# Kernel tuning notes

Hardware: AMD Instinct MI355X
Metric: run time of the kernel (lower is better)

The kernel has to match this reference:

```python
import jax, jax.numpy as jnp
import numpy as np

N, E, CIN, COUT, KHOP = 100000, 600000, 128, 128, 3


def setup_inputs() -> dict:
    key = jax.random.key(0)
    k1, k2, k3 = jax.random.split(key, 3)
    x = jax.random.normal(k1, (N, CIN), dtype=jnp.float32)
    edge_index = jax.random.randint(k2, (2, E), 0, N, dtype=jnp.int64)
    # xavier_uniform init for weight [in, out]
    limit = float(np.sqrt(6.0 / (CIN + COUT)))
    weight = jax.random.uniform(k3, (CIN, COUT), minval=-limit, maxval=limit, dtype=jnp.float32)
    bias = jnp.zeros((COUT,), jnp.float32)
    log_scale = jnp.asarray(np.log(1.0), jnp.float32)  # init_scale = 1.0
    hop_logits = jnp.zeros((KHOP + 1,), jnp.float32)
    return {"x": x, "edge_index": edge_index, "num_nodes": N,
            "weight": weight, "bias": bias,
            "log_scale": log_scale, "hop_logits": hop_logits}


def reference(x, edge_index, num_nodes, weight, bias, log_scale, hop_logits):
    src, dst = edge_index[0], edge_index[1]
    # symmetric normalization D_src^{-1/2} A D_dst^{-1/2}, no self-loops
    ones = jnp.ones(src.shape, x.dtype)
    deg_src = jax.ops.segment_sum(ones, src, num_segments=num_nodes)
    deg_dst = jax.ops.segment_sum(ones, dst, num_segments=num_nodes)
    dsi = jnp.where(deg_src > 0, jax.lax.rsqrt(jnp.maximum(deg_src, 1.0)), 0.0)
    ddi = jnp.where(deg_dst > 0, jax.lax.rsqrt(jnp.maximum(deg_dst, 1.0)), 0.0)
    edge_weight = dsi[src] * ddi[dst]  # [E]

    s = jnp.exp(log_scale)
    alpha = jax.nn.softmax(hop_logits)  # [k_hop+1]

    wavelet_out = alpha[0] * x
    current = x
    for k in range(1, KHOP + 1):  # small fixed hop count
        # A_hat @ current : gather -> scale -> scatter-add
        current = jax.ops.segment_sum(current[src] * edge_weight[:, None], dst,
                                      num_segments=num_nodes)
        decay = jnp.exp(-s * k)
        wavelet_out = wavelet_out + alpha[k] * decay * current

    return wavelet_out @ weight + bias
```

## Files before the change

### kernel.cpp

```cpp
#include <hip/hip_runtime.h>
#include <hip/hip_bf16.h>

#define C 128

typedef short s16x8 __attribute__((ext_vector_type(8)));
typedef float f32x4 __attribute__((ext_vector_type(4)));
typedef float f32x2 __attribute__((ext_vector_type(2)));

static __device__ __forceinline__ float b2f(unsigned short u) {
    union { unsigned int i; float f; } v;
    v.i = ((unsigned int)u) << 16;
    return v.f;
}
static __device__ __forceinline__ unsigned short f2b(float f) {
    __hip_bfloat16 b = __float2bfloat16(f);
    return *reinterpret_cast<unsigned short*>(&b);
}

__global__ __launch_bounds__(256) void zero_int_kernel(int4* __restrict__ p, long n4) {
    long i = blockIdx.x * 256L + threadIdx.x;
    if (i < n4) p[i] = make_int4(0, 0, 0, 0);
}

__global__ __launch_bounds__(256) void hist_kernel(
    const int* __restrict__ ei, int E,
    int* __restrict__ degs, int* __restrict__ degd) {
    int i = blockIdx.x * 256 + threadIdx.x;
    int e0 = i * 4;
    if (e0 + 4 <= E) {
        int4 s = *(const int4*)(ei + e0);
        int4 d = *(const int4*)(ei + E + e0);
        atomicAdd(&degs[s.x], 1); atomicAdd(&degs[s.y], 1);
        atomicAdd(&degs[s.z], 1); atomicAdd(&degs[s.w], 1);
        atomicAdd(&degd[d.x], 1); atomicAdd(&degd[d.y], 1);
        atomicAdd(&degd[d.z], 1); atomicAdd(&degd[d.w], 1);
    } else {
        for (int e = e0; e < E; ++e) {
            atomicAdd(&degs[ei[e]], 1);
            atomicAdd(&degd[ei[E + e]], 1);
        }
    }
}

__global__ __launch_bounds__(256) void wt_kernel(const float* __restrict__ W,
                                                 unsigned short* __restrict__ WtB,
                                                 const float* __restrict__ log_scale,
                                                 const float* __restrict__ hop_logits,
                                                 float* __restrict__ coef) {
    int tid = blockIdx.x * 256 + threadIdx.x;
    int k = tid & 127, c = tid >> 7;
    WtB[c * 128 + k] = f2b(W[k * 128 + c]);
    if (tid == 0) {
        float s = expf(log_scale[0]);
        float m = hop_logits[0];
        for (int kk = 1; kk < 4; ++kk) m = fmaxf(m, hop_logits[kk]);
        float a[4], sum = 0.0f;
        for (int kk = 0; kk < 4; ++kk) { a[kk] = expf(hop_logits[kk] - m); sum += a[kk]; }
        for (int kk = 0; kk < 4; ++kk) coef[kk] = (a[kk] / sum) * expf(-s * (float)kk);
    }
}

__global__ __launch_bounds__(256) void rpscan_kernel(const int* __restrict__ degd,
                                                     int* __restrict__ rp,
                                                     int* __restrict__ cursor,
                                                     int* __restrict__ gctr, int N) {
    __shared__ int sm[256];
    __shared__ int base_sm;
    int t = threadIdx.x;
    int i = blockIdx.x * 256 + t;
    int v = (i < N) ? degd[i] : 0;
    sm[t] = v;
    __syncthreads();
    for (int off = 1; off < 256; off <<= 1) {
        int add = (t >= off) ? sm[t - off] : 0;
        __syncthreads();
        sm[t] += add;
        __syncthreads();
    }
    if (t == 255) base_sm = atomicAdd(gctr, sm[255]);
    __syncthreads();
    if (i < N) {
        int r = base_sm + sm[t] - v;
        rp[i] = r;
        cursor[i] = r;
    }
}

__global__ __launch_bounds__(256) void scatter_kernel(const int* __restrict__ ei, int E,
                                                      int* __restrict__ cursor,
                                                      const int* __restrict__ degs,
                                                      int2* __restrict__ csr) {
    int i = blockIdx.x * 256 + threadIdx.x;
    int e0 = i * 4;
    if (e0 + 4 <= E) {
        int4 s = *(const int4*)(ei + e0);
        int4 d = *(const int4*)(ei + E + e0);
        float w0 = rsqrtf((float)degs[s.x]);
        float w1 = rsqrtf((float)degs[s.y]);
        float w2 = rsqrtf((float)degs[s.z]);
        float w3 = rsqrtf((float)degs[s.w]);
        int p0 = atomicAdd(&cursor[d.x], 1);
        int p1 = atomicAdd(&cursor[d.y], 1);
        int p2 = atomicAdd(&cursor[d.z], 1);
        int p3 = atomicAdd(&cursor[d.w], 1);
        csr[p0] = make_int2(s.x, __float_as_int(w0));
        csr[p1] = make_int2(s.y, __float_as_int(w1));
        csr[p2] = make_int2(s.z, __float_as_int(w2));
        csr[p3] = make_int2(s.w, __float_as_int(w3));
    } else {
        for (int e = e0; e < E; ++e) {
            int s = ei[e];
            int d = ei[E + e];
            float w = rsqrtf((float)degs[s]);
            int pos = atomicAdd(&cursor[d], 1);
            csr[pos] = make_int2(s, __float_as_int(w));
        }
    }
}

__global__ __launch_bounds__(256) void conv8_kernel(const float* __restrict__ x,
                                                    unsigned int* __restrict__ x8, long n4) {
    long i = blockIdx.x * 256L + threadIdx.x;
    if (i >= n4) return;
    float4 v = ((const float4*)x)[i];
    int r = __builtin_amdgcn_cvt_pk_fp8_f32(v.x, v.y, 0, false);
    r = __builtin_amdgcn_cvt_pk_fp8_f32(v.z, v.w, r, true);
    x8[i] = (unsigned int)r;
}

__global__ __launch_bounds__(256) void pull8_kernel(
    const int* __restrict__ rp, const int* __restrict__ degd,
    const int2* __restrict__ csr,
    const unsigned short* __restrict__ src8,
    unsigned short* __restrict__ dst8, int N) {
    int wid = (int)((blockIdx.x * 256L + threadIdx.x) >> 6);
    if (wid >= N) return;
    int lane = threadIdx.x & 63;
    int beg = __builtin_amdgcn_readfirstlane(rp[wid]);
    int cnt = __builtin_amdgcn_readfirstlane(degd[wid]);
    float sx = 0.f, sy = 0.f;
    if (cnt > 0) {
        for (int j = 0; j < cnt; j += 8) {
            int   idx[8];
            float wt[8];
            #pragma unroll
            for (int i = 0; i < 8; ++i) {
                int jj = j + i;
                bool ok = jj < cnt;
                int2 e = csr[beg + (ok ? jj : 0)];
                idx[i] = e.x;
                wt[i] = ok ? __int_as_float(e.y) : 0.0f;
            }
            unsigned short u[8];
            #pragma unroll
            for (int i = 0; i < 8; ++i) u[i] = src8[(long)idx[i] * 64 + lane];
            #pragma unroll
            for (int i = 0; i < 8; ++i) {
                f32x2 v = __builtin_amdgcn_cvt_pk_f32_fp8((int)u[i], false);
                sx += wt[i] * v[0];
                sy += wt[i] * v[1];
            }
        }
        float dv = rsqrtf((float)cnt);
        sx *= dv; sy *= dv;
    }
    int pk = __builtin_amdgcn_cvt_pk_fp8_f32(sx, sy, 0, false);
    dst8[(long)wid * 64 + lane] = (unsigned short)pk;
}

__global__ __launch_bounds__(256) void pull3c8_kernel(
    const int* __restrict__ rp, const int* __restrict__ degd,
    const int2* __restrict__ csr,
    const unsigned short* __restrict__ h2_8,
    const float* __restrict__ x,
    const unsigned short* __restrict__ h1_8,
    const float* __restrict__ coef,
    unsigned int* __restrict__ hc, int N) {
    int wid = (int)((blockIdx.x * 256L + threadIdx.x) >> 6);
    if (wid >= N) return;
    int lane = threadIdx.x & 63;
    int beg = __builtin_amdgcn_readfirstlane(rp[wid]);
    int cnt = __builtin_amdgcn_readfirstlane(degd[wid]);
    float sx = 0.f, sy = 0.f;
    if (cnt > 0) {
        for (int j = 0; j < cnt; j += 8) {
            int   idx[8];
            float wt[8];
            #pragma unroll
            for (int i = 0; i < 8; ++i) {
                int jj = j + i;
                bool ok = jj < cnt;
                int2 e = csr[beg + (ok ? jj : 0)];
                idx[i] = e.x;
                wt[i] = ok ? __int_as_float(e.y) : 0.0f;
            }
            unsigned short u[8];
            #pragma unroll
            for (int i = 0; i < 8; ++i) u[i] = h2_8[(long)idx[i] * 64 + lane];
            #pragma unroll
            for (int i = 0; i < 8; ++i) {
                f32x2 v = __builtin_amdgcn_cvt_pk_f32_fp8((int)u[i], false);
                sx += wt[i] * v[0];
                sy += wt[i] * v[1];
            }
        }
        float dv = rsqrtf((float)cnt);
        sx *= dv; sy *= dv;
    }
    float c0 = coef[0], c1 = coef[1], c2 = coef[2], c3 = coef[3];
    long rb = (long)wid * 64 + lane;
    float2 xv = *(const float2*)(x + (long)wid * C + lane * 2);
    f32x2 v1 = __builtin_amdgcn_cvt_pk_f32_fp8((int)h1_8[rb], false);
    f32x2 v2 = __builtin_amdgcn_cvt_pk_f32_fp8((int)h2_8[rb], false);
    float f0 = c0 * xv.x + c1 * v1[0] + c2 * v2[0] + c3 * sx;
    float f1 = c0 * xv.y + c1 * v1[1] + c2 * v2[1] + c3 * sy;
    hc[rb] = (unsigned int)f2b(f0) | ((unsigned int)f2b(f1) << 16);
}

__global__ __launch_bounds__(256) void gemm_kernel(
    const unsigned short* __restrict__ hc,
    const unsigned short* __restrict__ WtB,
    const float* __restrict__ bias,
    float* __restrict__ out, int N) {
    __shared__ unsigned short Wl[128 * 136];
    int t = threadIdx.x;

    #pragma unroll
    for (int i = 0; i < 8; ++i) {
        int ch = t + i * 256;
        int r = ch >> 4;
        int ko = (ch & 15) * 8;
        *(s16x8*)(Wl + r * 136 + ko) = *(const s16x8*)(WtB + r * 128 + ko);
    }
    __syncthreads();

    int wave = t >> 6, lane = t & 63;
    int lsel = lane & 15;
    int lk   = (lane >> 4) * 8;
    int arow = blockIdx.x * 64 + wave * 16 + lsel;
    bool rok = arow < N;
    long rbase = (long)arow * C;

    f32x4 acc[8];
    #pragma unroll
    for (int i = 0; i < 8; ++i) acc[i] = (f32x4){0.f, 0.f, 0.f, 0.f};

    #pragma unroll
    for (int ks = 0; ks < 4; ++ks) {
        int k0 = ks * 32 + lk;
        s16x8 a = rok ? *(const s16x8*)(hc + rbase + k0) : (s16x8)0;
        #pragma unroll
        for (int cf = 0; cf < 8; ++cf) {
            s16x8 b = *(const s16x8*)(Wl + (cf * 16 + lsel) * 136 + k0);
            acc[cf] = __builtin_amdgcn_mfma_f32_16x16x32_bf16(a, b, acc[cf], 0, 0, 0);
        }
    }

    int orow0 = blockIdx.x * 64 + wave * 16 + (lane >> 4) * 4;
    #pragma unroll
    for (int cf = 0; cf < 8; ++cf) {
        int ocol = cf * 16 + lsel;
        float bv = bias[ocol];
        #pragma unroll
        for (int r = 0; r < 4; ++r) {
            int orow = orow0 + r;
            if (orow < N) out[(long)orow * C + ocol] = acc[cf][r] + bv;
        }
    }
}

extern "C" void kernel_launch(void* const* d_in, const int* in_sizes, int n_in,
                              void* d_out, int out_size, void* d_ws, size_t ws_size,
                              hipStream_t stream) {
    const float* x          = (const float*)d_in[0];
    const int*   ei         = (const int*)d_in[1];
    const float* W          = (const float*)d_in[3];
    const float* bias       = (const float*)d_in[4];
    const float* log_scale  = (const float*)d_in[5];
    const float* hop_logits = (const float*)d_in[6];
    float* out = (float*)d_out;

    int N = in_sizes[0] / C;
    int E = in_sizes[1] / 2;

    char* ws = (char*)d_ws;
    size_t f8b = (size_t)N * C;
    unsigned short* x8  = (unsigned short*)ws;
    unsigned short* h18 = (unsigned short*)(ws + f8b);
    unsigned short* h28 = (unsigned short*)(ws + 2 * f8b);
    unsigned short* hc  = (unsigned short*)(ws + 3 * f8b);
    int2*  csr     = (int2*)(ws + 5 * f8b);
    int*   degs    = (int*)(csr + E);
    int*   degd    = degs + N;
    int*   gctr    = degd + N;
    int*   rp      = gctr + 16;
    int*   cursor  = rp + N;
    float* coef    = (float*)(cursor + N);
    unsigned short* WtB = (unsigned short*)(coef + 4);

    int eb4 = (E / 4 + 255) / 256 + 1;
    int nbk = (N + 255) / 256;
    int pull_blocks = (int)(((long)N * 64 + 255) / 256);

    long zn4 = (2L * N + 16 + 3) / 4;
    zero_int_kernel<<<(int)((zn4 + 255) / 256), 256, 0, stream>>>((int4*)degs, zn4);
    hist_kernel<<<eb4, 256, 0, stream>>>(ei, E, degs, degd);
    wt_kernel<<<64, 256, 0, stream>>>(W, WtB, log_scale, hop_logits, coef);
    rpscan_kernel<<<nbk, 256, 0, stream>>>(degd, rp, cursor, gctr, N);
    scatter_kernel<<<eb4, 256, 0, stream>>>(ei, E, cursor, degs, csr);

    long n4 = (long)N * C / 4;
    conv8_kernel<<<(int)((n4 + 255) / 256), 256, 0, stream>>>(x, (unsigned int*)x8, n4);

    pull8_kernel<<<pull_blocks, 256, 0, stream>>>(rp, degd, csr, x8,  h18, N);
    pull8_kernel<<<pull_blocks, 256, 0, stream>>>(rp, degd, csr, h18, h28, N);

    pull3c8_kernel<<<pull_blocks, 256, 0, stream>>>(rp, degd, csr, h28, x, h18, coef,
                                                    (unsigned int*)hc, N);

    gemm_kernel<<<(N + 63) / 64, 256, 0, stream>>>(hc, WtB, bias, out, N);
}
```

Before: 233.0 us.

## Fold source-degree scaling into node features and shrink CSR to index-only

The per-edge source normalisation weight moves out of the CSR and into the node features. Each pull now writes both the plain hop result and a copy pre-scaled by the source-degree factor, and the next hop gathers that scaled copy. The CSR entries drop from 8 bytes to 4, so edge-list traffic in the three pulls is halved. In exchange each pull writes an extra fp8 feature array, and the pre-scaling happens before fp8 quantisation, which changes rounding. The weight-transpose kernel is also merged into the conversion kernel to remove one launch.

After: 227.8 us. -2.2%, faster.

```diff
diff --git a/kernel.cpp b/kernel.cpp
--- a/kernel.cpp
+++ b/kernel.cpp
@@ -42,24 +42,6 @@
     }
 }
 
-__global__ __launch_bounds__(256) void wt_kernel(const float* __restrict__ W,
-                                                 unsigned short* __restrict__ WtB,
-                                                 const float* __restrict__ log_scale,
-                                                 const float* __restrict__ hop_logits,
-                                                 float* __restrict__ coef) {
-    int tid = blockIdx.x * 256 + threadIdx.x;
-    int k = tid & 127, c = tid >> 7;
-    WtB[c * 128 + k] = f2b(W[k * 128 + c]);
-    if (tid == 0) {
-        float s = expf(log_scale[0]);
-        float m = hop_logits[0];
-        for (int kk = 1; kk < 4; ++kk) m = fmaxf(m, hop_logits[kk]);
-        float a[4], sum = 0.0f;
-        for (int kk = 0; kk < 4; ++kk) { a[kk] = expf(hop_logits[kk] - m); sum += a[kk]; }
-        for (int kk = 0; kk < 4; ++kk) coef[kk] = (a[kk] / sum) * expf(-s * (float)kk);
-    }
-}
-
 __global__ __launch_bounds__(256) void rpscan_kernel(const int* __restrict__ degd,
                                                      int* __restrict__ rp,
                                                      int* __restrict__ cursor,
@@ -86,53 +68,69 @@
     }
 }
 
+__global__ __launch_bounds__(256) void conv8wt_kernel(
+    const float* __restrict__ x, const int* __restrict__ degs,
+    unsigned int* __restrict__ x8g, long n4,
+    const float* __restrict__ W, unsigned short* __restrict__ WtB,
+    const float* __restrict__ log_scale, const float* __restrict__ hop_logits,
+    float* __restrict__ coef, int convBlocks) {
+    if ((int)blockIdx.x >= convBlocks) {
+        int tid = ((int)blockIdx.x - convBlocks) * 256 + threadIdx.x;
+        int k = tid & 127, c = tid >> 7;
+        WtB[c * 128 + k] = f2b(W[k * 128 + c]);
+        if (tid == 0) {
+            float s = expf(log_scale[0]);
+            float m = hop_logits[0];
+            for (int kk = 1; kk < 4; ++kk) m = fmaxf(m, hop_logits[kk]);
+            float a[4], sum = 0.0f;
+            for (int kk = 0; kk < 4; ++kk) { a[kk] = expf(hop_logits[kk] - m); sum += a[kk]; }
+            for (int kk = 0; kk < 4; ++kk) coef[kk] = (a[kk] / sum) * expf(-s * (float)kk);
+        }
+        return;
+    }
+    long i = blockIdx.x * 256L + threadIdx.x;
+    if (i >= n4) return;
+    int n = (int)(i >> 5);
+    int od = degs[n];
+    float w = od > 0 ? rsqrtf((float)od) : 0.0f;
+    float4 v = ((const float4*)x)[i];
+    int r = __builtin_amdgcn_cvt_pk_fp8_f32(w * v.x, w * v.y, 0, false);
+    r = __builtin_amdgcn_cvt_pk_fp8_f32(w * v.z, w * v.w, r, true);
+    x8g[i] = (unsigned int)r;
+}
+
 __global__ __launch_bounds__(256) void scatter_kernel(const int* __restrict__ ei, int E,
                                                       int* __restrict__ cursor,
-                                                      const int* __restrict__ degs,
-                                                      int2* __restrict__ csr) {
+                                                      unsigned int* __restrict__ csrp) {
     int i = blockIdx.x * 256 + threadIdx.x;
     int e0 = i * 4;
     if (e0 + 4 <= E) {
         int4 s = *(const int4*)(ei + e0);
         int4 d = *(const int4*)(ei + E + e0);
-        float w0 = rsqrtf((float)degs[s.x]);
-        float w1 = rsqrtf((float)degs[s.y]);
-        float w2 = rsqrtf((float)degs[s.z]);
-        float w3 = rsqrtf((float)degs[s.w]);
         int p0 = atomicAdd(&cursor[d.x], 1);
         int p1 = atomicAdd(&cursor[d.y], 1);
         int p2 = atomicAdd(&cursor[d.z], 1);
         int p3 = atomicAdd(&cursor[d.w], 1);
-        csr[p0] = make_int2(s.x, __float_as_int(w0));
-        csr[p1] = make_int2(s.y, __float_as_int(w1));
-        csr[p2] = make_int2(s.z, __float_as_int(w2));
-        csr[p3] = make_int2(s.w, __float_as_int(w3));
+        csrp[p0] = (unsigned int)s.x;
+        csrp[p1] = (unsigned int)s.y;
+        csrp[p2] = (unsigned int)s.z;
+        csrp[p3] = (unsigned int)s.w;
     } else {
         for (int e = e0; e < E; ++e) {
             int s = ei[e];
             int d = ei[E + e];
-            float w = rsqrtf((float)degs[s]);
             int pos = atomicAdd(&cursor[d], 1);
-            csr[pos] = make_int2(s, __float_as_int(w));
-        }
-    }
-}
-
-__global__ __launch_bounds__(256) void conv8_kernel(const float* __restrict__ x,
-                                                    unsigned int* __restrict__ x8, long n4) {
-    long i = blockIdx.x * 256L + threadIdx.x;
-    if (i >= n4) return;
-    float4 v = ((const float4*)x)[i];
-    int r = __builtin_amdgcn_cvt_pk_fp8_f32(v.x, v.y, 0, false);
-    r = __builtin_amdgcn_cvt_pk_fp8_f32(v.z, v.w, r, true);
-    x8[i] = (unsigned int)r;
-}
-
-__global__ __launch_bounds__(256) void pull8_kernel(
+            csrp[pos] = (unsigned int)s;
+        }
+    }
+}
+
+__global__ __launch_bounds__(256) void pullg_kernel(
     const int* __restrict__ rp, const int* __restrict__ degd,
-    const int2* __restrict__ csr,
-    const unsigned short* __restrict__ src8,
-    unsigned short* __restrict__ dst8, int N) {
+    const int* __restrict__ degs,
+    const unsigned int* __restrict__ csrp,
+    const unsigned short* __restrict__ src_g,
+    unsigned short* __restrict__ h8, unsigned short* __restrict__ g8, int N) {
     int wid = (int)((blockIdx.x * 256L + threadIdx.x) >> 6);
     if (wid >= N) return;
     int lane = threadIdx.x & 63;
@@ -142,38 +140,41 @@
     if (cnt > 0) {
         for (int j = 0; j < cnt; j += 8) {
             int   idx[8];
-            float wt[8];
+            float mk[8];
             #pragma unroll
             for (int i = 0; i < 8; ++i) {
                 int jj = j + i;
                 bool ok = jj < cnt;
-                int2 e = csr[beg + (ok ? jj : 0)];
-                idx[i] = e.x;
-                wt[i] = ok ? __int_as_float(e.y) : 0.0f;
+                idx[i] = (int)csrp[beg + (ok ? jj : 0)];
+                mk[i] = ok ? 1.0f : 0.0f;
             }
             unsigned short u[8];
             #pragma unroll
-            for (int i = 0; i < 8; ++i) u[i] = src8[(long)idx[i] * 64 + lane];
+            for (int i = 0; i < 8; ++i) u[i] = src_g[(long)idx[i] * 64 + lane];
             #pragma unroll
             for (int i = 0; i < 8; ++i) {
                 f32x2 v = __builtin_amdgcn_cvt_pk_f32_fp8((int)u[i], false);
-                sx += wt[i] * v[0];
-                sy += wt[i] * v[1];
+                sx += mk[i] * v[0];
+                sy += mk[i] * v[1];
             }
         }
         float dv = rsqrtf((float)cnt);
         sx *= dv; sy *= dv;
     }
-    int pk = __builtin_amdgcn_cvt_pk_fp8_f32(sx, sy, 0, false);
-    dst8[(long)wid * 64 + lane] = (unsigned short)pk;
+    int od = __builtin_amdgcn_readfirstlane(degs[wid]);
+    float ds = od > 0 ? rsqrtf((float)od) : 0.0f;
+    long rb = (long)wid * 64 + lane;
+    h8[rb] = (unsigned short)__builtin_amdgcn_cvt_pk_fp8_f32(sx, sy, 0, false);
+    g8[rb] = (unsigned short)__builtin_amdgcn_cvt_pk_fp8_f32(ds * sx, ds * sy, 0, false);
 }
 
 __global__ __launch_bounds__(256) void pull3c8_kernel(
     const int* __restrict__ rp, const int* __restrict__ degd,
-    const int2* __restrict__ csr,
-    const unsigned short* __restrict__ h2_8,
+    const unsigned int* __restrict__ csrp,
+    const unsigned short* __restrict__ g2_8,
     const float* __restrict__ x,
     const unsigned short* __restrict__ h1_8,
+    const unsigned short* __restrict__ h2_8,
     const float* __restrict__ coef,
     unsigned int* __restrict__ hc, int N) {
     int wid = (int)((blockIdx.x * 256L + threadIdx.x) >> 6);
@@ -185,23 +186,22 @@
     if (cnt > 0) {
         for (int j = 0; j < cnt; j += 8) {
             int   idx[8];
-            float wt[8];
+            float mk[8];
             #pragma unroll
             for (int i = 0; i < 8; ++i) {
                 int jj = j + i;
                 bool ok = jj < cnt;
-                int2 e = csr[beg + (ok ? jj : 0)];
-                idx[i] = e.x;
-                wt[i] = ok ? __int_as_float(e.y) : 0.0f;
+                idx[i] = (int)csrp[beg + (ok ? jj : 0)];
+                mk[i] = ok ? 1.0f : 0.0f;
             }
             unsigned short u[8];
             #pragma unroll
-            for (int i = 0; i < 8; ++i) u[i] = h2_8[(long)idx[i] * 64 + lane];
+            for (int i = 0; i < 8; ++i) u[i] = g2_8[(long)idx[i] * 64 + lane];
             #pragma unroll
             for (int i = 0; i < 8; ++i) {
                 f32x2 v = __builtin_amdgcn_cvt_pk_f32_fp8((int)u[i], false);
-                sx += wt[i] * v[0];
-                sy += wt[i] * v[1];
+                sx += mk[i] * v[0];
+                sy += mk[i] * v[1];
             }
         }
         float dv = rsqrtf((float)cnt);
@@ -285,12 +285,14 @@
 
     char* ws = (char*)d_ws;
     size_t f8b = (size_t)N * C;
-    unsigned short* x8  = (unsigned short*)ws;
-    unsigned short* h18 = (unsigned short*)(ws + f8b);
-    unsigned short* h28 = (unsigned short*)(ws + 2 * f8b);
-    unsigned short* hc  = (unsigned short*)(ws + 3 * f8b);
-    int2*  csr     = (int2*)(ws + 5 * f8b);
-    int*   degs    = (int*)(csr + E);
+    unsigned short* x8g = (unsigned short*)ws;
+    unsigned short* g1  = (unsigned short*)(ws + f8b);
+    unsigned short* h1  = (unsigned short*)(ws + 2 * f8b);
+    unsigned short* g2  = (unsigned short*)(ws + 3 * f8b);
+    unsigned short* h2  = (unsigned short*)(ws + 4 * f8b);
+    unsigned short* hc  = (unsigned short*)(ws + 5 * f8b);
+    unsigned int* csrp  = (unsigned int*)(ws + 7 * f8b);
+    int*   degs    = (int*)(csrp + E);
     int*   degd    = degs + N;
     int*   gctr    = degd + N;
     int*   rp      = gctr + 16;
@@ -301,21 +303,22 @@
     int eb4 = (E / 4 + 255) / 256 + 1;
     int nbk = (N + 255) / 256;
     int pull_blocks = (int)(((long)N * 64 + 255) / 256);
+    long n4 = (long)N * C / 4;
+    int convBlocks = (int)((n4 + 255) / 256);
 
     long zn4 = (2L * N + 16 + 3) / 4;
     zero_int_kernel<<<(int)((zn4 + 255) / 256), 256, 0, stream>>>((int4*)degs, zn4);
     hist_kernel<<<eb4, 256, 0, stream>>>(ei, E, degs, degd);
-    wt_kernel<<<64, 256, 0, stream>>>(W, WtB, log_scale, hop_logits, coef);
     rpscan_kernel<<<nbk, 256, 0, stream>>>(degd, rp, cursor, gctr, N);
-    scatter_kernel<<<eb4, 256, 0, stream>>>(ei, E, cursor, degs, csr);
-
-    long n4 = (long)N * C / 4;
-    conv8_kernel<<<(int)((n4 + 255) / 256), 256, 0, stream>>>(x, (unsigned int*)x8, n4);
-
-    pull8_kernel<<<pull_blocks, 256, 0, stream>>>(rp, degd, csr, x8,  h18, N);
-    pull8_kernel<<<pull_blocks, 256, 0, stream>>>(rp, degd, csr, h18, h28, N);
-
-    pull3c8_kernel<<<pull_blocks, 256, 0, stream>>>(rp, degd, csr, h28, x, h18, coef,
+    conv8wt_kernel<<<convBlocks + 64, 256, 0, stream>>>(x, degs, (unsigned int*)x8g, n4,
+                                                        W, WtB, log_scale, hop_logits,
+                                                        coef, convBlocks);
+    scatter_kernel<<<eb4, 256, 0, stream>>>(ei, E, cursor, csrp);
+
+    pullg_kernel<<<pull_blocks, 256, 0, stream>>>(rp, degd, degs, csrp, x8g, h1, g1, N);
+    pullg_kernel<<<pull_blocks, 256, 0, stream>>>(rp, degd, degs, csrp, g1,  h2, g2, N);
+
+    pull3c8_kernel<<<pull_blocks, 256, 0, stream>>>(rp, degd, csrp, g2, x, h1, h2, coef,
                                                     (unsigned int*)hc, N);
 
     gemm_kernel<<<(N + 63) / 64, 256, 0, stream>>>(hc, WtB, bias, out, N);
```
